# Kernel tuning notes

Measured on AMD Instinct MI355X. Metric: run time of the kernel, lower is better.

Reference implementation:

```python
import jax, jax.numpy as jnp
import numpy as np

HIDDEN = 896
INTER = 2560
N_EXPERTS = 16
TOP_K = 4


def setup_inputs() -> dict:
    key = jax.random.key(0)
    ks = jax.random.split(key, 9)
    s = lambda fan_in: 1.0 / np.sqrt(fan_in)
    x = jax.random.normal(ks[0], (2, 1024, HIDDEN), dtype=jnp.float32)
    router_w = jax.random.normal(ks[1], (HIDDEN, N_EXPERTS), dtype=jnp.float32) * s(HIDDEN)
    # routed experts, stacked: y = x @ W (equivalent to nn.Linear with W.T)
    Wg = jax.random.normal(ks[2], (N_EXPERTS, HIDDEN, INTER), dtype=jnp.float32) * s(HIDDEN)
    Wu = jax.random.normal(ks[3], (N_EXPERTS, HIDDEN, INTER), dtype=jnp.float32) * s(HIDDEN)
    Wd = jax.random.normal(ks[4], (N_EXPERTS, INTER, HIDDEN), dtype=jnp.float32) * s(INTER)
    # single shared expert
    Sg = jax.random.normal(ks[5], (HIDDEN, INTER), dtype=jnp.float32) * s(HIDDEN)
    Su = jax.random.normal(ks[6], (HIDDEN, INTER), dtype=jnp.float32) * s(HIDDEN)
    Sd = jax.random.normal(ks[7], (INTER, HIDDEN), dtype=jnp.float32) * s(INTER)
    return {"x": x, "router_w": router_w, "Wg": Wg, "Wu": Wu, "Wd": Wd,
            "Sg": Sg, "Su": Su, "Sd": Sd}


def reference(x, router_w, Wg, Wu, Wd, Sg, Su, Sd):
    B, N, D = x.shape
    xf = x.reshape(-1, D)  # [T, D]

    # shared expert (all tokens): SwiGLU
    shared = (jax.nn.silu(xf @ Sg) * (xf @ Su)) @ Sd  # [T, D]

    # router: softmax -> top-k -> renormalize
    logits = xf @ router_w                      # [T, E]
    probs = jax.nn.softmax(logits, axis=-1)
    top_v, top_i = jax.lax.top_k(probs, TOP_K)  # [T, K]
    w = top_v / (top_v.sum(axis=-1, keepdims=True) + 1e-8)

    # load-balance loss
    one_hot = jax.nn.one_hot(top_i, N_EXPERTS, dtype=probs.dtype)  # [T, K, E]
    f = one_hot.sum(axis=1).mean(axis=0)   # fraction routed per expert
    P = probs.mean(axis=0)                 # mean router prob per expert
    balance_loss = N_EXPERTS * (f * P).sum()

    # dense-dispatch combine weights [T, E] (zero for unselected experts)
    combine = (w[..., None] * one_hot).sum(axis=1)  # [T, E]

    # all-expert SwiGLU, combined with per-token routing weights
    g = jnp.einsum('td,edi->tei', xf, Wg)
    u = jnp.einsum('td,edi->tei', xf, Wu)
    h = jax.nn.silu(g) * u                          # [T, E, I]
    routed = jnp.einsum('tei,eid,te->td', h, Wd, combine)

    out = (routed + shared).reshape(B, N, D)
    return out, balance_loss
```

## Files before the change

### kernel.cpp

```cpp
#include <hip/hip_runtime.h>
#include <hip/hip_bf16.h>


#define T_TOK 2048
#define DIM   896
#define INTERN 2560
#define NEXP  16
#define TOPK  4
#define MT    64
#define IC    256
#define ICAP  133

#define SLOTGU ((size_t)80 * 56 * 512)
#define SLOTD  ((size_t)28 * 160 * 512)

typedef __attribute__((ext_vector_type(8)))  __bf16 bf16x8;
typedef __attribute__((ext_vector_type(4)))  __bf16 bf16x4;
typedef __attribute__((ext_vector_type(16))) float  f32x16;

__device__ __forceinline__ void panel_barrier() {
  asm volatile("s_waitcnt lgkmcnt(0)" ::: "memory");
  __builtin_amdgcn_s_barrier();
  __builtin_amdgcn_sched_barrier(0);
}

__device__ __forceinline__ bool decode_work(const int* cnt, int b, int idx,
                                            int& g, int& tile) {
  int K0 = (cnt[b] + MT - 1) >> 6;
  int K1 = (cnt[b + 8] + MT - 1) >> 6;
  if (idx < K0) { g = b; tile = idx; return true; }
  idx -= K0;
  if (idx < K1) { g = b + 8; tile = idx; return true; }
  idx -= K1;
  if (idx < 4) { g = NEXP; tile = b + 8 * idx; return true; }
  return false;
}

__global__ void router_k(const float* __restrict__ x, const float* __restrict__ rw,
                         int* __restrict__ cnt, float* __restrict__ Pacc,
                         float* __restrict__ facc, int* __restrict__ tok,
                         float* __restrict__ wts) {
  int lane = threadIdx.x & 63;
  int t = blockIdx.x * 4 + (threadIdx.x >> 6);
  const float* xr = x + (size_t)t * DIM;

  float acc[NEXP];
#pragma unroll
  for (int e = 0; e < NEXP; ++e) acc[e] = 0.f;
  for (int i = 0; i < DIM / 64; ++i) {
    int d = i * 64 + lane;
    float xv = xr[d];
    const float* r = rw + d * NEXP;
#pragma unroll
    for (int e = 0; e < NEXP; ++e) acc[e] = fmaf(xv, r[e], acc[e]);
  }
#pragma unroll
  for (int e = 0; e < NEXP; ++e) {
    float v = acc[e];
    v += __shfl_xor(v, 32); v += __shfl_xor(v, 16); v += __shfl_xor(v, 8);
    v += __shfl_xor(v, 4);  v += __shfl_xor(v, 2);  v += __shfl_xor(v, 1);
    acc[e] = v;
  }
  float m = acc[0];
#pragma unroll
  for (int e = 1; e < NEXP; ++e) m = fmaxf(m, acc[e]);
  float p[NEXP]; float s = 0.f;
#pragma unroll
  for (int e = 0; e < NEXP; ++e) { p[e] = __expf(acc[e] - m); s += p[e]; }
  float is = 1.f / s;
#pragma unroll
  for (int e = 0; e < NEXP; ++e) p[e] *= is;

  float pc[NEXP];
#pragma unroll
  for (int e = 0; e < NEXP; ++e) pc[e] = p[e];
  int sels[TOPK]; float svs[TOPK]; float s4 = 0.f;
#pragma unroll
  for (int k = 0; k < TOPK; ++k) {
    int best = 0; float bv = pc[0];
#pragma unroll
    for (int e = 1; e < NEXP; ++e) { if (pc[e] > bv) { bv = pc[e]; best = e; } }
    sels[k] = best; svs[k] = bv; s4 += bv;
#pragma unroll
    for (int e = 0; e < NEXP; ++e) { if (e == best) pc[e] = -1.f; }
  }
  float inv = 1.f / (s4 + 1e-8f);

  if (lane < NEXP) atomicAdd(&Pacc[lane], p[lane] * (1.f / T_TOK));
  if (lane < TOPK) {
    int e = sels[lane]; float w = svs[lane] * inv;
    atomicAdd(&facc[e], 1.f / T_TOK);
    int pos = atomicAdd(&cnt[e], 1);
    tok[e * T_TOK + pos] = t;
    wts[e * T_TOK + pos] = w;
  }
}

__global__ void loss_k(const float* __restrict__ Pacc, const float* __restrict__ facc,
                       const int* __restrict__ cnt, int* __restrict__ offs,
                       float* __restrict__ dst) {
  if (threadIdx.x == 0) {
    float s = 0.f;
    for (int e = 0; e < NEXP; ++e) s += Pacc[e] * facc[e];
    *dst = (float)NEXP * s;
    int o = 0;
    for (int e = 0; e < NEXP; ++e) { offs[e] = o; o += cnt[e]; }
    offs[NEXP] = o;
  }
}

__global__ __launch_bounds__(256, 8) void packall_k(
    const float* __restrict__ Wg, const float* __restrict__ Sg,
    __hip_bfloat16* __restrict__ PG,
    const float* __restrict__ Wu, const float* __restrict__ Su,
    __hip_bfloat16* __restrict__ PU,
    const float* __restrict__ Wd, const float* __restrict__ Sd,
    __hip_bfloat16* __restrict__ PD) {
  int bid = blockIdx.x;
  int which = bid / 9520;
  int r = bid % 9520;
  int z = r / 560, rr = r % 560;
  int K, N, kt, nt;
  const float *srcE, *srcS; __hip_bfloat16* dst;
  if (which < 2) {
    K = DIM; N = INTERN; kt = rr % 14; nt = rr / 14;
    srcE = which ? Wu : Wg; srcS = which ? Su : Sg; dst = which ? PU : PG;
  } else {
    K = INTERN; N = DIM; kt = rr % 40; nt = rr / 40;
    srcE = Wd; srcS = Sd; dst = PD;
  }
  const float* src = (z < NEXP) ? srcE + (size_t)z * K * N : srcS;
  __hip_bfloat16* d = dst + (size_t)z * ((size_t)(K >> 4) * (N >> 5) * 512);

  __shared__ float tile[64][65];
  int tid = threadIdx.x;
  int r0 = tid >> 4, c4 = (tid & 15) << 2;
  const float* s = src + (size_t)(kt * 64) * N + nt * 64;
#pragma unroll
  for (int it = 0; it < 4; ++it) {
    int rw_ = r0 + 16 * it;
    float4 v = *reinterpret_cast<const float4*>(s + (size_t)rw_ * N + c4);
    tile[rw_][c4] = v.x; tile[rw_][c4 + 1] = v.y;
    tile[rw_][c4 + 2] = v.z; tile[rw_][c4 + 3] = v.w;
  }
  __syncthreads();
  int lane = tid & 63, h5 = lane >> 5, c31 = lane & 31;
  int KS = K >> 4;
#pragma unroll
  for (int it = 0; it < 2; ++it) {
    int cc = (tid >> 6) + 4 * it;
    int nbl = cc >> 2, ksl = cc & 3;
    bf16x8 v;
#pragma unroll
    for (int e = 0; e < 8; ++e)
      v[e] = (__bf16)tile[ksl * 16 + 8 * h5 + e][nbl * 32 + c31];
    size_t n_blk = (size_t)nt * 2 + nbl, ks = (size_t)kt * 4 + ksl;
    *reinterpret_cast<bf16x8*>(d + ((n_blk * KS + ks) * 64 + lane) * 8) = v;
  }
}

__global__ __launch_bounds__(512, 4) void h4_k(
    const float* __restrict__ x, const int* __restrict__ cnt,
    const int* __restrict__ offs, const int* __restrict__ tok,
    const __hip_bfloat16* __restrict__ PG, const __hip_bfloat16* __restrict__ PU,
    __hip_bfloat16* __restrict__ H) {
  int bid = blockIdx.x;
  int ch = bid / (8 * ICAP);
  int r_ = bid % (8 * ICAP);
  int b = r_ & 7, idx = r_ >> 3;
  int g, tile;
  if (!decode_work(cnt, b, idx, g, tile)) return;
  int M = (g < NEXP) ? cnt[g] : T_TOK;
  int m0 = tile * MT;

  __shared__ int rows_s[MT];
  __shared__ __align__(16) char xph[32768];
  char (*xp)[16384] = reinterpret_cast<char (*)[16384]>(xph);
  char* hb = xph;

  int tid = threadIdx.x;
  if (tid < MT) {
    if (g < NEXP) {
      int i = m0 + tid;
      rows_s[tid] = tok[g * T_TOK + ((i < M) ? i : m0)];
    } else rows_s[tid] = m0 + tid;
  }
  __syncthreads();

  int wv = tid >> 6, lane = tid & 63;
  int h5 = lane >> 5, c31 = lane & 31;

  int srow = tid >> 3, sc8 = tid & 7;
  const float* xr = x + (size_t)rows_s[srow] * DIM;
  int sswz = (srow & 7) << 4;

#define LDX(p, j) (*reinterpret_cast<const float4*>(xr + (p) * 128 + (sc8 + 8 * (j)) * 4))
#define STX(pb, j, v) { bf16x4 _b; _b[0]=(__bf16)(v).x; _b[1]=(__bf16)(v).y; \
    _b[2]=(__bf16)(v).z; _b[3]=(__bf16)(v).w; \
    *reinterpret_cast<bf16x4*>(&xp[pb][(srow * 256 + sc8 * 8 + 64 * (j)) ^ sswz]) = _b; }
#define XF(pb, row, ksl) (*reinterpret_cast<const bf16x8*>( \
    &xp[pb][((row) * 256 + (ksl) * 32 + h5 * 16) ^ (((row) & 7) << 4)]))

  int slot = (g < NEXP) ? g : NEXP;
  const __hip_bfloat16* bg = PG + (size_t)slot * SLOTGU +
      ((size_t)(ch * 8 + wv) * 56) * 512 + lane * 8;
  const __hip_bfloat16* bu = PU + (size_t)slot * SLOTGU +
      ((size_t)(ch * 8 + wv) * 56) * 512 + lane * 8;

  bf16x8 g0 = *reinterpret_cast<const bf16x8*>(bg);
  bf16x8 g1 = *reinterpret_cast<const bf16x8*>(bg + 512);
  bf16x8 g2 = *reinterpret_cast<const bf16x8*>(bg + 1024);
  bf16x8 g3 = *reinterpret_cast<const bf16x8*>(bg + 1536);
  bf16x8 u0 = *reinterpret_cast<const bf16x8*>(bu);
  bf16x8 u1 = *reinterpret_cast<const bf16x8*>(bu + 512);
  bf16x8 u2 = *reinterpret_cast<const bf16x8*>(bu + 1024);
  bf16x8 u3 = *reinterpret_cast<const bf16x8*>(bu + 1536);

  {
    float4 a0 = LDX(0, 0), a1 = LDX(0, 1), a2 = LDX(0, 2), a3 = LDX(0, 3);
    STX(0, 0, a0) STX(0, 1, a1) STX(0, 2, a2) STX(0, 3, a3)
  }
  panel_barrier();

  f32x16 ag0, ag1, au0, au1;
#pragma unroll
  for (int r = 0; r < 16; ++r) { ag0[r] = 0.f; ag1[r] = 0.f; au0[r] = 0.f; au1[r] = 0.f; }

#define STEP(S, GB, UB) { \
    bf16x8 xa = XF(pb, c31, S), xb = XF(pb, c31 + 32, S); \
    ag0 = __builtin_amdgcn_mfma_f32_32x32x16_bf16(GB, xa, ag0, 0, 0, 0); \
    ag1 = __builtin_amdgcn_mfma_f32_32x32x16_bf16(GB, xb, ag1, 0, 0, 0); \
    au0 = __builtin_amdgcn_mfma_f32_32x32x16_bf16(UB, xa, au0, 0, 0, 0); \
    au1 = __builtin_amdgcn_mfma_f32_32x32x16_bf16(UB, xb, au1, 0, 0, 0); \
    int nk = 8 * p + (S) + 4; if (nk >= 56) nk = 0; \
    GB = *reinterpret_cast<const bf16x8*>(bg + (size_t)nk * 512); \
    UB = *reinterpret_cast<const bf16x8*>(bu + (size_t)nk * 512); }

  float4 s0, s1, s2, s3;
  for (int p = 0; p < 7; ++p) {
    int pb = p & 1;
    if (p < 6) { s0 = LDX(p + 1, 0); s1 = LDX(p + 1, 1); }
    STEP(0, g0, u0) STEP(1, g1, u1) STEP(2, g2, u2)
    if (p < 6) {
      STX(pb ^ 1, 0, s0) STX(pb ^ 1, 1, s1)
      s2 = LDX(p + 1, 2); s3 = LDX(p + 1, 3);
    }
    STEP(3, g3, u3) STEP(4, g0, u0) STEP(5, g1, u1)
    if (p < 6) { STX(pb ^ 1, 2, s2) STX(pb ^ 1, 3, s3) }
    STEP(6, g2, u2) STEP(7, g3, u3)
    panel_barrier();
  }
#undef STEP

#pragma unroll
  for (int mh = 0; mh < 2; ++mh) {
    int tokr = c31 + 32 * mh;
#pragma unroll
    for (int q = 0; q < 4; ++q) {
      bf16x4 hq;
#pragma unroll
      for (int j = 0; j < 4; ++j) {
        float gg = mh ? ag1[4 * q + j] : ag0[4 * q + j];
        float uu = mh ? au1[4 * q + j] : au0[4 * q + j];
        hq[j] = (__bf16)(gg / (1.f + __expf(-gg)) * uu);
      }
      int i0 = wv * 32 + 8 * q + 4 * h5;
      int byte = (tokr * 512 + i0 * 2) ^ ((tokr & 7) << 4);
      *reinterpret_cast<bf16x4*>(&hb[byte]) = hq;
    }
  }
  panel_barrier();

  if (g == NEXP || m0 + srow < M) {
    int slotr = offs[g] + m0 + srow;
    __hip_bfloat16* hrow = H + (size_t)slotr * INTERN + ch * IC + sc8 * 32;
#pragma unroll
    for (int qq = 0; qq < 4; ++qq) {
      int byte = (srow * 512 + sc8 * 64 + qq * 16) ^ sswz;
      *reinterpret_cast<bf16x8*>(hrow + qq * 8) =
          *reinterpret_cast<const bf16x8*>(&hb[byte]);
    }
  }
#undef LDX
#undef STX
#undef XF
}

__global__ __launch_bounds__(512, 4) void g24_k(
    const int* __restrict__ cnt, const int* __restrict__ offs,
    const int* __restrict__ tok, const float* __restrict__ wts,
    const __hip_bfloat16* __restrict__ H,
    const __hip_bfloat16* __restrict__ PD, float* __restrict__ out) {
  int bid = blockIdx.x;
  int ns = bid / (8 * ICAP);
  int r_ = bid % (8 * ICAP);
  int b = r_ & 7, idx = r_ >> 3;
  int g, tile;
  if (!decode_work(cnt, b, idx, g, tile)) return;
  int M = (g < NEXP) ? cnt[g] : T_TOK;
  int m0 = tile * MT;

  __shared__ int rows_s[MT];
  __shared__ float w_s[MT];
  __shared__ __align__(16) char hp[2][16384];

  int tid = threadIdx.x;
  if (tid < MT) {
    if (g < NEXP) {
      int i = m0 + tid; bool v = i < M;
      rows_s[tid] = tok[g * T_TOK + (v ? i : m0)];
      w_s[tid]   = v ? wts[g * T_TOK + i] : 0.f;
    } else { rows_s[tid] = m0 + tid; w_s[tid] = 1.f; }
  }
  __syncthreads();

  int wv = tid >> 6, lane = tid & 63, h5 = lane >> 5, c31 = lane & 31;
  int mh = wv & 1, ng = wv >> 1;
  int col = ns * 128 + ng * 32 + c31;

  int slot = (g < NEXP) ? g : NEXP;
  const __hip_bfloat16* bd = PD + (size_t)slot * SLOTD +
      ((size_t)(ns * 4 + ng) * 160) * 512 + lane * 8;

  int slot0 = offs[g] + m0;
  const __hip_bfloat16* Hb = H + (size_t)slot0 * INTERN;

  int srow = tid >> 3, sc8 = tid & 7;
  const __hip_bfloat16* hr = Hb + (size_t)srow * INTERN + sc8 * 16;
  int sswz = (srow & 7) << 4;

  bf16x8 w0 = *reinterpret_cast<const bf16x8*>(bd);
  bf16x8 w1 = *reinterpret_cast<const bf16x8*>(bd + 512);
  bf16x8 w2 = *reinterpret_cast<const bf16x8*>(bd + 1024);
  bf16x8 w3 = *reinterpret_cast<const bf16x8*>(bd + 1536);
  bf16x8 w4 = *reinterpret_cast<const bf16x8*>(bd + 2048);
  bf16x8 w5 = *reinterpret_cast<const bf16x8*>(bd + 2560);
  bf16x8 w6 = *reinterpret_cast<const bf16x8*>(bd + 3072);
  bf16x8 w7 = *reinterpret_cast<const bf16x8*>(bd + 3584);

  bf16x8 t0 = *reinterpret_cast<const bf16x8*>(hr);
  bf16x8 t1 = *reinterpret_cast<const bf16x8*>(hr + 8);
  {
    int b0 = srow * 256 + sc8 * 32;
    *reinterpret_cast<bf16x8*>(&hp[0][b0 ^ sswz]) = t0;
    *reinterpret_cast<bf16x8*>(&hp[0][(b0 + 16) ^ sswz]) = t1;
  }
  panel_barrier();

  f32x16 o;
#pragma unroll
  for (int r = 0; r < 16; ++r) o[r] = 0.f;

  int arow = mh * 32 + c31;
  int aswz = (arow & 7) << 4;

#define G2STEP(KSL, WB) { \
    bf16x8 hf = *reinterpret_cast<const bf16x8*>( \
        &hp[pb][(arow * 256 + (KSL) * 32 + h5 * 16) ^ aswz]); \
    o = __builtin_amdgcn_mfma_f32_32x32x16_bf16(hf, WB, o, 0, 0, 0); \
    int tn = 8 * p + (KSL) + 8; if (tn >= 160) tn -= 160; \
    WB = *reinterpret_cast<const bf16x8*>(bd + (size_t)tn * 512); }

  for (int p = 0; p < 20; ++p) {
    int pb = p & 1;
    if (p < 19) {
      t0 = *reinterpret_cast<const bf16x8*>(hr + (p + 1) * 128);
      t1 = *reinterpret_cast<const bf16x8*>(hr + (p + 1) * 128 + 8);
    }
    G2STEP(0, w0) G2STEP(1, w1) G2STEP(2, w2) G2STEP(3, w3)
    G2STEP(4, w4) G2STEP(5, w5) G2STEP(6, w6) G2STEP(7, w7)
    if (p < 19) {
      int b0 = srow * 256 + sc8 * 32;
      *reinterpret_cast<bf16x8*>(&hp[pb ^ 1][b0 ^ sswz]) = t0;
      *reinterpret_cast<bf16x8*>(&hp[pb ^ 1][(b0 + 16) ^ sswz]) = t1;
    }
    panel_barrier();
  }
#undef G2STEP

#pragma unroll
  for (int r = 0; r < 16; ++r) {
    int row = (r & 3) + 8 * (r >> 2) + 4 * h5 + 32 * mh;
    atomicAdd(&out[(size_t)rows_s[row] * DIM + col], o[r] * w_s[row]);
  }
}

extern "C" void kernel_launch(void* const* d_in, const int* in_sizes, int n_in,
                              void* d_out, int out_size, void* d_ws, size_t ws_size,
                              hipStream_t stream) {
  const float* x  = (const float*)d_in[0];
  const float* rw = (const float*)d_in[1];
  const float* Wg = (const float*)d_in[2];
  const float* Wu = (const float*)d_in[3];
  const float* Wd = (const float*)d_in[4];
  const float* Sg = (const float*)d_in[5];
  const float* Su = (const float*)d_in[6];
  const float* Sd = (const float*)d_in[7];
  float* out = (float*)d_out;

  char* ws = (char*)d_ws;
  int*   cnt  = (int*)ws;
  float* Pacc = (float*)(ws + 64);
  float* facc = (float*)(ws + 128);
  int*   offs = (int*)(ws + 192);
  int*   tok  = (int*)(ws + 320);
  float* wts  = (float*)(ws + 320 + 131072);
  const size_t H_OFF = 262656;
  __hip_bfloat16* H = (__hip_bfloat16*)(ws + H_OFF);
  const size_t H_BYTES = (size_t)(2 * T_TOK * TOPK + T_TOK) * INTERN * 2;

  const size_t PG_OFF = H_OFF + H_BYTES;
  const size_t PBYTES = (size_t)17 * SLOTGU * 2;
  const size_t PU_OFF = PG_OFF + PBYTES;
  const size_t PD_OFF = PU_OFF + PBYTES;
  __hip_bfloat16* PG = (__hip_bfloat16*)(ws + PG_OFF);
  __hip_bfloat16* PU = (__hip_bfloat16*)(ws + PU_OFF);
  __hip_bfloat16* PD = (__hip_bfloat16*)(ws + PD_OFF);

  hipMemsetAsync(d_ws, 0, 320, stream);
  hipMemsetAsync(d_out, 0, (size_t)(T_TOK * DIM + 1) * sizeof(float), stream);

  router_k<<<T_TOK / 4, 256, 0, stream>>>(x, rw, cnt, Pacc, facc, tok, wts);
  loss_k<<<1, 64, 0, stream>>>(Pacc, facc, cnt, offs, out + (size_t)T_TOK * DIM);
  packall_k<<<28560, 256, 0, stream>>>(Wg, Sg, PG, Wu, Su, PU, Wd, Sd, PD);
  h4_k<<<10 * 8 * ICAP, 512, 0, stream>>>(x, cnt, offs, tok, PG, PU, H);
  g24_k<<<7 * 8 * ICAP, 512, 0, stream>>>(cnt, offs, tok, wts, H, PD, out);
}
```

Baseline: 539.7 us.

## Stream gate/up weights through LDS via direct global-to-LDS loads

The gate/up kernel now loads packed weight fragments with global_load_lds into double-buffered LDS instead of register prefetch. The x panel is restaged in 32-column chunks with padded rows rather than a swizzle. The K loop goes from 7 panels of 8 k-steps to 28 panels of 2 k-steps, with a full vmcnt wait and a barrier every panel. This frees registers and lets the hardware copy weights directly into LDS. In exchange it adds many more barriers, shallower prefetch, and LDS use rises to about 75KB per block, which may limit occupancy.

```diff
diff --git a/kernel.cpp b/kernel.cpp
--- a/kernel.cpp
+++ b/kernel.cpp
@@ -17,6 +17,10 @@
 typedef __attribute__((ext_vector_type(8)))  __bf16 bf16x8;
 typedef __attribute__((ext_vector_type(4)))  __bf16 bf16x4;
 typedef __attribute__((ext_vector_type(16))) float  f32x16;
+
+#define GLD_LDS(GP, LP) __builtin_amdgcn_global_load_lds( \
+    (const __attribute__((address_space(1))) void*)(GP), \
+    (__attribute__((address_space(3))) void*)(LP), 16, 0, 0)
 
 __device__ __forceinline__ void panel_barrier() {
   asm volatile("s_waitcnt lgkmcnt(0)" ::: "memory");
@@ -159,7 +163,7 @@
   }
 }
 
-__global__ __launch_bounds__(512, 4) void h4_k(
+__global__ __launch_bounds__(512, 4) void h5_k(
     const float* __restrict__ x, const int* __restrict__ cnt,
     const int* __restrict__ offs, const int* __restrict__ tok,
     const __hip_bfloat16* __restrict__ PG, const __hip_bfloat16* __restrict__ PU,
@@ -174,9 +178,9 @@
   int m0 = tile * MT;
 
   __shared__ int rows_s[MT];
-  __shared__ __align__(16) char xph[32768];
-  char (*xp)[16384] = reinterpret_cast<char (*)[16384]>(xph);
-  char* hb = xph;
+  __shared__ __align__(16) char wb[2][32768];
+  __shared__ __align__(16) char xb[2][5120];
+  char* hb = &wb[0][0];
 
   int tid = threadIdx.x;
   if (tid < MT) {
@@ -189,17 +193,8 @@
 
   int wv = tid >> 6, lane = tid & 63;
   int h5 = lane >> 5, c31 = lane & 31;
-
   int srow = tid >> 3, sc8 = tid & 7;
   const float* xr = x + (size_t)rows_s[srow] * DIM;
-  int sswz = (srow & 7) << 4;
-
-#define LDX(p, j) (*reinterpret_cast<const float4*>(xr + (p) * 128 + (sc8 + 8 * (j)) * 4))
-#define STX(pb, j, v) { bf16x4 _b; _b[0]=(__bf16)(v).x; _b[1]=(__bf16)(v).y; \
-    _b[2]=(__bf16)(v).z; _b[3]=(__bf16)(v).w; \
-    *reinterpret_cast<bf16x4*>(&xp[pb][(srow * 256 + sc8 * 8 + 64 * (j)) ^ sswz]) = _b; }
-#define XF(pb, row, ksl) (*reinterpret_cast<const bf16x8*>( \
-    &xp[pb][((row) * 256 + (ksl) * 32 + h5 * 16) ^ (((row) & 7) << 4)]))
 
   int slot = (g < NEXP) ? g : NEXP;
   const __hip_bfloat16* bg = PG + (size_t)slot * SLOTGU +
@@ -207,50 +202,55 @@
   const __hip_bfloat16* bu = PU + (size_t)slot * SLOTGU +
       ((size_t)(ch * 8 + wv) * 56) * 512 + lane * 8;
 
-  bf16x8 g0 = *reinterpret_cast<const bf16x8*>(bg);
-  bf16x8 g1 = *reinterpret_cast<const bf16x8*>(bg + 512);
-  bf16x8 g2 = *reinterpret_cast<const bf16x8*>(bg + 1024);
-  bf16x8 g3 = *reinterpret_cast<const bf16x8*>(bg + 1536);
-  bf16x8 u0 = *reinterpret_cast<const bf16x8*>(bu);
-  bf16x8 u1 = *reinterpret_cast<const bf16x8*>(bu + 512);
-  bf16x8 u2 = *reinterpret_cast<const bf16x8*>(bu + 1024);
-  bf16x8 u3 = *reinterpret_cast<const bf16x8*>(bu + 1536);
-
-  {
-    float4 a0 = LDX(0, 0), a1 = LDX(0, 1), a2 = LDX(0, 2), a3 = LDX(0, 3);
-    STX(0, 0, a0) STX(0, 1, a1) STX(0, 2, a2) STX(0, 3, a3)
-  }
+#define ISSUE_W(PB, P) { \
+    char* wdst = &wb[PB][wv * 4096]; \
+    const __hip_bfloat16* gg_ = bg + (size_t)(2 * (P)) * 512; \
+    const __hip_bfloat16* gu_ = bu + (size_t)(2 * (P)) * 512; \
+    GLD_LDS(gg_,       wdst); \
+    GLD_LDS(gg_ + 512, wdst + 1024); \
+    GLD_LDS(gu_,       wdst + 2048); \
+    GLD_LDS(gu_ + 512, wdst + 3072); }
+
+#define KSTEP(PB, KSL) { \
+    bf16x8 wg = *reinterpret_cast<const bf16x8*>(&wb[PB][wv * 4096 + (KSL) * 1024 + lane * 16]); \
+    bf16x8 wu = *reinterpret_cast<const bf16x8*>(&wb[PB][wv * 4096 + 2048 + (KSL) * 1024 + lane * 16]); \
+    bf16x8 xa = *reinterpret_cast<const bf16x8*>(&xb[PB][c31 * 80 + (KSL) * 32 + h5 * 16]); \
+    bf16x8 xc = *reinterpret_cast<const bf16x8*>(&xb[PB][(c31 + 32) * 80 + (KSL) * 32 + h5 * 16]); \
+    ag0 = __builtin_amdgcn_mfma_f32_32x32x16_bf16(wg, xa, ag0, 0, 0, 0); \
+    ag1 = __builtin_amdgcn_mfma_f32_32x32x16_bf16(wg, xc, ag1, 0, 0, 0); \
+    au0 = __builtin_amdgcn_mfma_f32_32x32x16_bf16(wu, xa, au0, 0, 0, 0); \
+    au1 = __builtin_amdgcn_mfma_f32_32x32x16_bf16(wu, xc, au1, 0, 0, 0); }
+
+#define STX_X(PB, V) { bf16x4 b4_; \
+    b4_[0] = (__bf16)(V).x; b4_[1] = (__bf16)(V).y; \
+    b4_[2] = (__bf16)(V).z; b4_[3] = (__bf16)(V).w; \
+    *reinterpret_cast<bf16x4*>(&xb[PB][srow * 80 + sc8 * 8]) = b4_; }
+
+  f32x16 ag0, ag1, au0, au1;
+#pragma unroll
+  for (int r = 0; r < 16; ++r) { ag0[r] = 0.f; ag1[r] = 0.f; au0[r] = 0.f; au1[r] = 0.f; }
+
+  float4 xv;
+  ISSUE_W(0, 0)
+  xv = *reinterpret_cast<const float4*>(xr + sc8 * 4);
+  asm volatile("s_waitcnt vmcnt(0)" ::: "memory");
+  STX_X(0, xv)
   panel_barrier();
 
-  f32x16 ag0, ag1, au0, au1;
-#pragma unroll
-  for (int r = 0; r < 16; ++r) { ag0[r] = 0.f; ag1[r] = 0.f; au0[r] = 0.f; au1[r] = 0.f; }
-
-#define STEP(S, GB, UB) { \
-    bf16x8 xa = XF(pb, c31, S), xb = XF(pb, c31 + 32, S); \
-    ag0 = __builtin_amdgcn_mfma_f32_32x32x16_bf16(GB, xa, ag0, 0, 0, 0); \
-    ag1 = __builtin_amdgcn_mfma_f32_32x32x16_bf16(GB, xb, ag1, 0, 0, 0); \
-    au0 = __builtin_amdgcn_mfma_f32_32x32x16_bf16(UB, xa, au0, 0, 0, 0); \
-    au1 = __builtin_amdgcn_mfma_f32_32x32x16_bf16(UB, xb, au1, 0, 0, 0); \
-    int nk = 8 * p + (S) + 4; if (nk >= 56) nk = 0; \
-    GB = *reinterpret_cast<const bf16x8*>(bg + (size_t)nk * 512); \
-    UB = *reinterpret_cast<const bf16x8*>(bu + (size_t)nk * 512); }
-
-  float4 s0, s1, s2, s3;
-  for (int p = 0; p < 7; ++p) {
+  for (int p = 0; p < 28; ++p) {
     int pb = p & 1;
-    if (p < 6) { s0 = LDX(p + 1, 0); s1 = LDX(p + 1, 1); }
-    STEP(0, g0, u0) STEP(1, g1, u1) STEP(2, g2, u2)
-    if (p < 6) {
-      STX(pb ^ 1, 0, s0) STX(pb ^ 1, 1, s1)
-      s2 = LDX(p + 1, 2); s3 = LDX(p + 1, 3);
+    if (p < 27) {
+      ISSUE_W(pb ^ 1, p + 1)
+      xv = *reinterpret_cast<const float4*>(xr + (p + 1) * 32 + sc8 * 4);
     }
-    STEP(3, g3, u3) STEP(4, g0, u0) STEP(5, g1, u1)
-    if (p < 6) { STX(pb ^ 1, 2, s2) STX(pb ^ 1, 3, s3) }
-    STEP(6, g2, u2) STEP(7, g3, u3)
+    KSTEP(pb, 0) KSTEP(pb, 1)
+    asm volatile("s_waitcnt vmcnt(0)" ::: "memory");
+    if (p < 27) STX_X(pb ^ 1, xv)
     panel_barrier();
   }
-#undef STEP
+#undef ISSUE_W
+#undef KSTEP
+#undef STX_X
 
 #pragma unroll
   for (int mh = 0; mh < 2; ++mh) {
@@ -273,6 +273,7 @@
 
   if (g == NEXP || m0 + srow < M) {
     int slotr = offs[g] + m0 + srow;
+    int sswz = (srow & 7) << 4;
     __hip_bfloat16* hrow = H + (size_t)slotr * INTERN + ch * IC + sc8 * 32;
 #pragma unroll
     for (int qq = 0; qq < 4; ++qq) {
@@ -281,9 +282,6 @@
           *reinterpret_cast<const bf16x8*>(&hb[byte]);
     }
   }
-#undef LDX
-#undef STX
-#undef XF
 }
 
 __global__ __launch_bounds__(512, 4) void g24_k(
@@ -423,6 +421,6 @@
   router_k<<<T_TOK / 4, 256, 0, stream>>>(x, rw, cnt, Pacc, facc, tok, wts);
   loss_k<<<1, 64, 0, stream>>>(Pacc, facc, cnt, offs, out + (size_t)T_TOK * DIM);
   packall_k<<<28560, 256, 0, stream>>>(Wg, Sg, PG, Wu, Su, PU, Wd, Sd, PD);
-  h4_k<<<10 * 8 * ICAP, 512, 0, stream>>>(x, cnt, offs, tok, PG, PU, H);
+  h5_k<<<10 * 8 * ICAP, 512, 0, stream>>>(x, cnt, offs, tok, PG, PU, H);
   g24_k<<<7 * 8 * ICAP, 512, 0, stream>>>(cnt, offs, tok, wts, H, PD, out);
 }
```

Measured after the change: 547.8 us. No clear change (+1.5%).

## Retile expert GEMMs to 128-token tiles with narrower intermediate chunks

Applied to the files above, without the earlier changes.

Both expert GEMM kernels now process 128-token tiles instead of 64. Waves are split into two token halves, and the gate/up kernel covers 128 intermediate columns per block instead of 256. The aim is to reuse each packed weight fragment across twice as many tokens, which halves weight traffic per token. The cost is more registers per wave (occupancy bound lowered to 3), more padding waste on partially filled expert tiles, and more K iterations each with a barrier.

```diff
diff --git a/kernel.cpp b/kernel.cpp
--- a/kernel.cpp
+++ b/kernel.cpp
@@ -7,9 +7,8 @@
 #define INTERN 2560
 #define NEXP  16
 #define TOPK  4
-#define MT    64
-#define IC    256
-#define ICAP  133
+#define MT    128
+#define ICAP  37
 
 #define SLOTGU ((size_t)80 * 56 * 512)
 #define SLOTD  ((size_t)28 * 160 * 512)
@@ -17,6 +16,15 @@
 typedef __attribute__((ext_vector_type(8)))  __bf16 bf16x8;
 typedef __attribute__((ext_vector_type(4)))  __bf16 bf16x4;
 typedef __attribute__((ext_vector_type(16))) float  f32x16;
+
+#define MFMA32(A, B, C) __builtin_amdgcn_mfma_f32_32x32x16_bf16(A, B, C, 0, 0, 0)
+
+__device__ __forceinline__ bf16x8 pack8(float4 a, float4 b) {
+  bf16x8 r;
+  r[0] = (__bf16)a.x; r[1] = (__bf16)a.y; r[2] = (__bf16)a.z; r[3] = (__bf16)a.w;
+  r[4] = (__bf16)b.x; r[5] = (__bf16)b.y; r[6] = (__bf16)b.z; r[7] = (__bf16)b.w;
+  return r;
+}
 
 __device__ __forceinline__ void panel_barrier() {
   asm volatile("s_waitcnt lgkmcnt(0)" ::: "memory");
@@ -26,13 +34,13 @@
 
 __device__ __forceinline__ bool decode_work(const int* cnt, int b, int idx,
                                             int& g, int& tile) {
-  int K0 = (cnt[b] + MT - 1) >> 6;
-  int K1 = (cnt[b + 8] + MT - 1) >> 6;
+  int K0 = (cnt[b] + MT - 1) >> 7;
+  int K1 = (cnt[b + 8] + MT - 1) >> 7;
   if (idx < K0) { g = b; tile = idx; return true; }
   idx -= K0;
   if (idx < K1) { g = b + 8; tile = idx; return true; }
   idx -= K1;
-  if (idx < 4) { g = NEXP; tile = b + 8 * idx; return true; }
+  if (idx < 2) { g = NEXP; tile = b + 8 * idx; return true; }
   return false;
 }
 
@@ -159,7 +167,7 @@
   }
 }
 
-__global__ __launch_bounds__(512, 4) void h4_k(
+__global__ __launch_bounds__(512, 3) void h8_k(
     const float* __restrict__ x, const int* __restrict__ cnt,
     const int* __restrict__ offs, const int* __restrict__ tok,
     const __hip_bfloat16* __restrict__ PG, const __hip_bfloat16* __restrict__ PU,
@@ -189,36 +197,46 @@
 
   int wv = tid >> 6, lane = tid & 63;
   int h5 = lane >> 5, c31 = lane & 31;
-
-  int srow = tid >> 3, sc8 = tid & 7;
+  int ig = wv & 3, th = wv >> 2;
+
+  int srow = tid >> 2, sc4 = tid & 3;
   const float* xr = x + (size_t)rows_s[srow] * DIM;
   int sswz = (srow & 7) << 4;
 
-#define LDX(p, j) (*reinterpret_cast<const float4*>(xr + (p) * 128 + (sc8 + 8 * (j)) * 4))
-#define STX(pb, j, v) { bf16x4 _b; _b[0]=(__bf16)(v).x; _b[1]=(__bf16)(v).y; \
-    _b[2]=(__bf16)(v).z; _b[3]=(__bf16)(v).w; \
-    *reinterpret_cast<bf16x4*>(&xp[pb][(srow * 256 + sc8 * 8 + 64 * (j)) ^ sswz]) = _b; }
+#define LDX(p, j) (*reinterpret_cast<const float4*>(xr + (p) * 64 + sc4 * 16 + (j) * 4))
+#define STXA(pb, v0, v1) { \
+    *reinterpret_cast<bf16x8*>(&xp[pb][(srow * 128 + sc4 * 32) ^ sswz]) = pack8(v0, v1); }
+#define STXB(pb, v2, v3) { \
+    *reinterpret_cast<bf16x8*>(&xp[pb][(srow * 128 + sc4 * 32 + 16) ^ sswz]) = pack8(v2, v3); }
 #define XF(pb, row, ksl) (*reinterpret_cast<const bf16x8*>( \
-    &xp[pb][((row) * 256 + (ksl) * 32 + h5 * 16) ^ (((row) & 7) << 4)]))
+    &xp[pb][((row) * 128 + (ksl) * 32 + h5 * 16) ^ (((row) & 7) << 4)]))
 
   int slot = (g < NEXP) ? g : NEXP;
   const __hip_bfloat16* bg = PG + (size_t)slot * SLOTGU +
-      ((size_t)(ch * 8 + wv) * 56) * 512 + lane * 8;
+      ((size_t)(ch * 4 + ig) * 56) * 512 + lane * 8;
   const __hip_bfloat16* bu = PU + (size_t)slot * SLOTGU +
-      ((size_t)(ch * 8 + wv) * 56) * 512 + lane * 8;
+      ((size_t)(ch * 4 + ig) * 56) * 512 + lane * 8;
 
   bf16x8 g0 = *reinterpret_cast<const bf16x8*>(bg);
   bf16x8 g1 = *reinterpret_cast<const bf16x8*>(bg + 512);
   bf16x8 g2 = *reinterpret_cast<const bf16x8*>(bg + 1024);
   bf16x8 g3 = *reinterpret_cast<const bf16x8*>(bg + 1536);
+  bf16x8 g4 = *reinterpret_cast<const bf16x8*>(bg + 2048);
+  bf16x8 g5 = *reinterpret_cast<const bf16x8*>(bg + 2560);
+  bf16x8 g6 = *reinterpret_cast<const bf16x8*>(bg + 3072);
+  bf16x8 g7 = *reinterpret_cast<const bf16x8*>(bg + 3584);
   bf16x8 u0 = *reinterpret_cast<const bf16x8*>(bu);
   bf16x8 u1 = *reinterpret_cast<const bf16x8*>(bu + 512);
   bf16x8 u2 = *reinterpret_cast<const bf16x8*>(bu + 1024);
   bf16x8 u3 = *reinterpret_cast<const bf16x8*>(bu + 1536);
+  bf16x8 u4 = *reinterpret_cast<const bf16x8*>(bu + 2048);
+  bf16x8 u5 = *reinterpret_cast<const bf16x8*>(bu + 2560);
+  bf16x8 u6 = *reinterpret_cast<const bf16x8*>(bu + 3072);
+  bf16x8 u7 = *reinterpret_cast<const bf16x8*>(bu + 3584);
 
   {
     float4 a0 = LDX(0, 0), a1 = LDX(0, 1), a2 = LDX(0, 2), a3 = LDX(0, 3);
-    STX(0, 0, a0) STX(0, 1, a1) STX(0, 2, a2) STX(0, 3, a3)
+    STXA(0, a0, a1) STXB(0, a2, a3)
   }
   panel_barrier();
 
@@ -227,45 +245,46 @@
   for (int r = 0; r < 16; ++r) { ag0[r] = 0.f; ag1[r] = 0.f; au0[r] = 0.f; au1[r] = 0.f; }
 
 #define STEP(S, GB, UB) { \
-    bf16x8 xa = XF(pb, c31, S), xb = XF(pb, c31 + 32, S); \
-    ag0 = __builtin_amdgcn_mfma_f32_32x32x16_bf16(GB, xa, ag0, 0, 0, 0); \
-    ag1 = __builtin_amdgcn_mfma_f32_32x32x16_bf16(GB, xb, ag1, 0, 0, 0); \
-    au0 = __builtin_amdgcn_mfma_f32_32x32x16_bf16(UB, xa, au0, 0, 0, 0); \
-    au1 = __builtin_amdgcn_mfma_f32_32x32x16_bf16(UB, xb, au1, 0, 0, 0); \
-    int nk = 8 * p + (S) + 4; if (nk >= 56) nk = 0; \
+    bf16x8 xa = XF(pb, th * 64 + c31, S), xb = XF(pb, th * 64 + 32 + c31, S); \
+    ag0 = MFMA32(GB, xa, ag0); ag1 = MFMA32(GB, xb, ag1); \
+    au0 = MFMA32(UB, xa, au0); au1 = MFMA32(UB, xb, au1); \
+    int nk = 4 * p + (S) + 8; if (nk >= 56) nk = 0; \
     GB = *reinterpret_cast<const bf16x8*>(bg + (size_t)nk * 512); \
     UB = *reinterpret_cast<const bf16x8*>(bu + (size_t)nk * 512); }
 
   float4 s0, s1, s2, s3;
-  for (int p = 0; p < 7; ++p) {
+  for (int p = 0; p < 14; ++p) {
     int pb = p & 1;
-    if (p < 6) { s0 = LDX(p + 1, 0); s1 = LDX(p + 1, 1); }
-    STEP(0, g0, u0) STEP(1, g1, u1) STEP(2, g2, u2)
-    if (p < 6) {
-      STX(pb ^ 1, 0, s0) STX(pb ^ 1, 1, s1)
+    if (p < 13) { s0 = LDX(p + 1, 0); s1 = LDX(p + 1, 1); }
+    if (p & 1) { STEP(0, g4, u4) STEP(1, g5, u5) }
+    else       { STEP(0, g0, u0) STEP(1, g1, u1) }
+    if (p < 13) {
       s2 = LDX(p + 1, 2); s3 = LDX(p + 1, 3);
-    }
-    STEP(3, g3, u3) STEP(4, g0, u0) STEP(5, g1, u1)
-    if (p < 6) { STX(pb ^ 1, 2, s2) STX(pb ^ 1, 3, s3) }
-    STEP(6, g2, u2) STEP(7, g3, u3)
+      STXA(pb ^ 1, s0, s1)
+    }
+    if (p & 1) { STEP(2, g6, u6) }
+    else       { STEP(2, g2, u2) }
+    if (p < 13) STXB(pb ^ 1, s2, s3)
+    if (p & 1) { STEP(3, g7, u7) }
+    else       { STEP(3, g3, u3) }
     panel_barrier();
   }
 #undef STEP
 
 #pragma unroll
-  for (int mh = 0; mh < 2; ++mh) {
-    int tokr = c31 + 32 * mh;
+  for (int tgl = 0; tgl < 2; ++tgl) {
+    int tokr = th * 64 + tgl * 32 + c31;
 #pragma unroll
     for (int q = 0; q < 4; ++q) {
       bf16x4 hq;
 #pragma unroll
       for (int j = 0; j < 4; ++j) {
-        float gg = mh ? ag1[4 * q + j] : ag0[4 * q + j];
-        float uu = mh ? au1[4 * q + j] : au0[4 * q + j];
+        float gg = tgl ? ag1[4 * q + j] : ag0[4 * q + j];
+        float uu = tgl ? au1[4 * q + j] : au0[4 * q + j];
         hq[j] = (__bf16)(gg / (1.f + __expf(-gg)) * uu);
       }
-      int i0 = wv * 32 + 8 * q + 4 * h5;
-      int byte = (tokr * 512 + i0 * 2) ^ ((tokr & 7) << 4);
+      int i0 = ig * 32 + 8 * q + 4 * h5;
+      int byte = (tokr * 256 + i0 * 2) ^ ((tokr & 7) << 4);
       *reinterpret_cast<bf16x4*>(&hb[byte]) = hq;
     }
   }
@@ -273,20 +292,21 @@
 
   if (g == NEXP || m0 + srow < M) {
     int slotr = offs[g] + m0 + srow;
-    __hip_bfloat16* hrow = H + (size_t)slotr * INTERN + ch * IC + sc8 * 32;
+    __hip_bfloat16* hrow = H + (size_t)slotr * INTERN + ch * 128 + sc4 * 32;
 #pragma unroll
     for (int qq = 0; qq < 4; ++qq) {
-      int byte = (srow * 512 + sc8 * 64 + qq * 16) ^ sswz;
+      int byte = (srow * 256 + sc4 * 64 + qq * 16) ^ sswz;
       *reinterpret_cast<bf16x8*>(hrow + qq * 8) =
           *reinterpret_cast<const bf16x8*>(&hb[byte]);
     }
   }
 #undef LDX
-#undef STX
+#undef STXA
+#undef STXB
 #undef XF
 }
 
-__global__ __launch_bounds__(512, 4) void g24_k(
+__global__ __launch_bounds__(512, 3) void g28_k(
     const int* __restrict__ cnt, const int* __restrict__ offs,
     const int* __restrict__ tok, const float* __restrict__ wts,
     const __hip_bfloat16* __restrict__ H,
@@ -315,18 +335,16 @@
   __syncthreads();
 
   int wv = tid >> 6, lane = tid & 63, h5 = lane >> 5, c31 = lane & 31;
-  int mh = wv & 1, ng = wv >> 1;
-  int col = ns * 128 + ng * 32 + c31;
+  int cg = wv & 3, th = wv >> 2;
+  int col = ns * 128 + cg * 32 + c31;
 
   int slot = (g < NEXP) ? g : NEXP;
   const __hip_bfloat16* bd = PD + (size_t)slot * SLOTD +
-      ((size_t)(ns * 4 + ng) * 160) * 512 + lane * 8;
+      ((size_t)(ns * 4 + cg) * 160) * 512 + lane * 8;
 
   int slot0 = offs[g] + m0;
-  const __hip_bfloat16* Hb = H + (size_t)slot0 * INTERN;
-
-  int srow = tid >> 3, sc8 = tid & 7;
-  const __hip_bfloat16* hr = Hb + (size_t)srow * INTERN + sc8 * 16;
+  int srow = tid >> 2, sc4 = tid & 3;
+  const __hip_bfloat16* hr = H + (size_t)(slot0 + srow) * INTERN + sc4 * 16;
   int sswz = (srow & 7) << 4;
 
   bf16x8 w0 = *reinterpret_cast<const bf16x8*>(bd);
@@ -341,47 +359,54 @@
   bf16x8 t0 = *reinterpret_cast<const bf16x8*>(hr);
   bf16x8 t1 = *reinterpret_cast<const bf16x8*>(hr + 8);
   {
-    int b0 = srow * 256 + sc8 * 32;
+    int b0 = srow * 128 + sc4 * 32;
     *reinterpret_cast<bf16x8*>(&hp[0][b0 ^ sswz]) = t0;
     *reinterpret_cast<bf16x8*>(&hp[0][(b0 + 16) ^ sswz]) = t1;
   }
   panel_barrier();
 
-  f32x16 o;
-#pragma unroll
-  for (int r = 0; r < 16; ++r) o[r] = 0.f;
-
-  int arow = mh * 32 + c31;
-  int aswz = (arow & 7) << 4;
-
-#define G2STEP(KSL, WB) { \
-    bf16x8 hf = *reinterpret_cast<const bf16x8*>( \
-        &hp[pb][(arow * 256 + (KSL) * 32 + h5 * 16) ^ aswz]); \
-    o = __builtin_amdgcn_mfma_f32_32x32x16_bf16(hf, WB, o, 0, 0, 0); \
-    int tn = 8 * p + (KSL) + 8; if (tn >= 160) tn -= 160; \
+  f32x16 o0, o1;
+#pragma unroll
+  for (int r = 0; r < 16; ++r) { o0[r] = 0.f; o1[r] = 0.f; }
+
+#define HPF(pb, row, ksl) (*reinterpret_cast<const bf16x8*>( \
+    &hp[pb][((row) * 128 + (ksl) * 32 + h5 * 16) ^ (((row) & 7) << 4)]))
+
+#define G2STEP(S, WB) { \
+    bf16x8 ha = HPF(pb, th * 64 + c31, S); \
+    bf16x8 hc = HPF(pb, th * 64 + 32 + c31, S); \
+    o0 = MFMA32(ha, WB, o0); o1 = MFMA32(hc, WB, o1); \
+    int tn = 4 * p + (S) + 8; if (tn >= 160) tn = 0; \
     WB = *reinterpret_cast<const bf16x8*>(bd + (size_t)tn * 512); }
 
-  for (int p = 0; p < 20; ++p) {
+  for (int p = 0; p < 40; ++p) {
     int pb = p & 1;
-    if (p < 19) {
-      t0 = *reinterpret_cast<const bf16x8*>(hr + (p + 1) * 128);
-      t1 = *reinterpret_cast<const bf16x8*>(hr + (p + 1) * 128 + 8);
-    }
-    G2STEP(0, w0) G2STEP(1, w1) G2STEP(2, w2) G2STEP(3, w3)
-    G2STEP(4, w4) G2STEP(5, w5) G2STEP(6, w6) G2STEP(7, w7)
-    if (p < 19) {
-      int b0 = srow * 256 + sc8 * 32;
+    if (p < 39) {
+      t0 = *reinterpret_cast<const bf16x8*>(hr + (p + 1) * 64);
+      t1 = *reinterpret_cast<const bf16x8*>(hr + (p + 1) * 64 + 8);
+    }
+    if (p & 1) { G2STEP(0, w4) G2STEP(1, w5) }
+    else       { G2STEP(0, w0) G2STEP(1, w1) }
+    if (p < 39) {
+      int b0 = srow * 128 + sc4 * 32;
       *reinterpret_cast<bf16x8*>(&hp[pb ^ 1][b0 ^ sswz]) = t0;
       *reinterpret_cast<bf16x8*>(&hp[pb ^ 1][(b0 + 16) ^ sswz]) = t1;
     }
+    if (p & 1) { G2STEP(2, w6) G2STEP(3, w7) }
+    else       { G2STEP(2, w2) G2STEP(3, w3) }
     panel_barrier();
   }
 #undef G2STEP
-
-#pragma unroll
-  for (int r = 0; r < 16; ++r) {
-    int row = (r & 3) + 8 * (r >> 2) + 4 * h5 + 32 * mh;
-    atomicAdd(&out[(size_t)rows_s[row] * DIM + col], o[r] * w_s[row]);
+#undef HPF
+
+#pragma unroll
+  for (int tgl = 0; tgl < 2; ++tgl) {
+#pragma unroll
+    for (int r = 0; r < 16; ++r) {
+      int row = th * 64 + tgl * 32 + (r & 3) + 8 * (r >> 2) + 4 * h5;
+      float v = (tgl ? o1[r] : o0[r]) * w_s[row];
+      atomicAdd(&out[(size_t)rows_s[row] * DIM + col], v);
+    }
   }
 }
 
@@ -423,6 +448,6 @@
   router_k<<<T_TOK / 4, 256, 0, stream>>>(x, rw, cnt, Pacc, facc, tok, wts);
   loss_k<<<1, 64, 0, stream>>>(Pacc, facc, cnt, offs, out + (size_t)T_TOK * DIM);
   packall_k<<<28560, 256, 0, stream>>>(Wg, Sg, PG, Wu, Su, PU, Wd, Sd, PD);
-  h4_k<<<10 * 8 * ICAP, 512, 0, stream>>>(x, cnt, offs, tok, PG, PU, H);
-  g24_k<<<7 * 8 * ICAP, 512, 0, stream>>>(cnt, offs, tok, wts, H, PD, out);
-}
+  h8_k<<<20 * 8 * ICAP, 512, 0, stream>>>(x, cnt, offs, tok, PG, PU, H);
+  g28_k<<<7 * 8 * ICAP, 512, 0, stream>>>(cnt, offs, tok, wts, H, PD, out);
+}
```

After: 1.568 ms. 190% more time.

## Make gate/up kernel weight-stationary with LDS-resident weight slices looping over all tokens

Applied to the files above, without the earlier changes.

The gate/up projection kernel is restructured so that each block owns one expert and one 32-column slice of the intermediate dimension. It loads the full 896x32 gate and up weight panels into LDS once, then loops over that expert's tokens in tiles of 256. This replaces the old layout, where many 64-token tiles each reread the weights from global memory, and is meant to cut repeated weight traffic. In exchange the launch drops to 1360 blocks of 256 threads using about 150KB of LDS, so occupancy is one block per CU. Each token tile also converts x to bf16 in a serialized panel loop with two barriers per panel, and blocks for heavily loaded experts run longer, which risks load imbalance.

```diff
diff --git a/kernel.cpp b/kernel.cpp
--- a/kernel.cpp
+++ b/kernel.cpp
@@ -8,7 +8,6 @@
 #define NEXP  16
 #define TOPK  4
 #define MT    64
-#define IC    256
 #define ICAP  133
 
 #define SLOTGU ((size_t)80 * 56 * 512)
@@ -17,6 +16,15 @@
 typedef __attribute__((ext_vector_type(8)))  __bf16 bf16x8;
 typedef __attribute__((ext_vector_type(4)))  __bf16 bf16x4;
 typedef __attribute__((ext_vector_type(16))) float  f32x16;
+
+#define MFMA32(A, B, C) __builtin_amdgcn_mfma_f32_32x32x16_bf16(A, B, C, 0, 0, 0)
+
+__device__ __forceinline__ bf16x8 pack8(float4 a, float4 b) {
+  bf16x8 r;
+  r[0] = (__bf16)a.x; r[1] = (__bf16)a.y; r[2] = (__bf16)a.z; r[3] = (__bf16)a.w;
+  r[4] = (__bf16)b.x; r[5] = (__bf16)b.y; r[6] = (__bf16)b.z; r[7] = (__bf16)b.w;
+  return r;
+}
 
 __device__ __forceinline__ void panel_barrier() {
   asm volatile("s_waitcnt lgkmcnt(0)" ::: "memory");
@@ -159,131 +167,106 @@
   }
 }
 
-__global__ __launch_bounds__(512, 4) void h4_k(
+__global__ __launch_bounds__(256, 1) void h9_k(
     const float* __restrict__ x, const int* __restrict__ cnt,
     const int* __restrict__ offs, const int* __restrict__ tok,
     const __hip_bfloat16* __restrict__ PG, const __hip_bfloat16* __restrict__ PU,
     __hip_bfloat16* __restrict__ H) {
   int bid = blockIdx.x;
-  int ch = bid / (8 * ICAP);
-  int r_ = bid % (8 * ICAP);
-  int b = r_ & 7, idx = r_ >> 3;
-  int g, tile;
-  if (!decode_work(cnt, b, idx, g, tile)) return;
+  int g = bid % 17, nc = bid / 17;
   int M = (g < NEXP) ? cnt[g] : T_TOK;
-  int m0 = tile * MT;
-
-  __shared__ int rows_s[MT];
-  __shared__ __align__(16) char xph[32768];
-  char (*xp)[16384] = reinterpret_cast<char (*)[16384]>(xph);
-  char* hb = xph;
+
+  __shared__ int rows_s[256];
+  __shared__ __align__(16) char wg[57344];
+  __shared__ __align__(16) char wu[57344];
+  __shared__ __align__(16) char xpan[32768];
 
   int tid = threadIdx.x;
-  if (tid < MT) {
-    if (g < NEXP) {
-      int i = m0 + tid;
-      rows_s[tid] = tok[g * T_TOK + ((i < M) ? i : m0)];
-    } else rows_s[tid] = m0 + tid;
-  }
-  __syncthreads();
-
   int wv = tid >> 6, lane = tid & 63;
   int h5 = lane >> 5, c31 = lane & 31;
-
-  int srow = tid >> 3, sc8 = tid & 7;
-  const float* xr = x + (size_t)rows_s[srow] * DIM;
-  int sswz = (srow & 7) << 4;
-
-#define LDX(p, j) (*reinterpret_cast<const float4*>(xr + (p) * 128 + (sc8 + 8 * (j)) * 4))
-#define STX(pb, j, v) { bf16x4 _b; _b[0]=(__bf16)(v).x; _b[1]=(__bf16)(v).y; \
-    _b[2]=(__bf16)(v).z; _b[3]=(__bf16)(v).w; \
-    *reinterpret_cast<bf16x4*>(&xp[pb][(srow * 256 + sc8 * 8 + 64 * (j)) ^ sswz]) = _b; }
-#define XF(pb, row, ksl) (*reinterpret_cast<const bf16x8*>( \
-    &xp[pb][((row) * 256 + (ksl) * 32 + h5 * 16) ^ (((row) & 7) << 4)]))
-
-  int slot = (g < NEXP) ? g : NEXP;
-  const __hip_bfloat16* bg = PG + (size_t)slot * SLOTGU +
-      ((size_t)(ch * 8 + wv) * 56) * 512 + lane * 8;
-  const __hip_bfloat16* bu = PU + (size_t)slot * SLOTGU +
-      ((size_t)(ch * 8 + wv) * 56) * 512 + lane * 8;
-
-  bf16x8 g0 = *reinterpret_cast<const bf16x8*>(bg);
-  bf16x8 g1 = *reinterpret_cast<const bf16x8*>(bg + 512);
-  bf16x8 g2 = *reinterpret_cast<const bf16x8*>(bg + 1024);
-  bf16x8 g3 = *reinterpret_cast<const bf16x8*>(bg + 1536);
-  bf16x8 u0 = *reinterpret_cast<const bf16x8*>(bu);
-  bf16x8 u1 = *reinterpret_cast<const bf16x8*>(bu + 512);
-  bf16x8 u2 = *reinterpret_cast<const bf16x8*>(bu + 1024);
-  bf16x8 u3 = *reinterpret_cast<const bf16x8*>(bu + 1536);
+  int wbase = wv * 64;
 
   {
-    float4 a0 = LDX(0, 0), a1 = LDX(0, 1), a2 = LDX(0, 2), a3 = LDX(0, 3);
-    STX(0, 0, a0) STX(0, 1, a1) STX(0, 2, a2) STX(0, 3, a3)
-  }
-  panel_barrier();
-
-  f32x16 ag0, ag1, au0, au1;
-#pragma unroll
-  for (int r = 0; r < 16; ++r) { ag0[r] = 0.f; ag1[r] = 0.f; au0[r] = 0.f; au1[r] = 0.f; }
-
-#define STEP(S, GB, UB) { \
-    bf16x8 xa = XF(pb, c31, S), xb = XF(pb, c31 + 32, S); \
-    ag0 = __builtin_amdgcn_mfma_f32_32x32x16_bf16(GB, xa, ag0, 0, 0, 0); \
-    ag1 = __builtin_amdgcn_mfma_f32_32x32x16_bf16(GB, xb, ag1, 0, 0, 0); \
-    au0 = __builtin_amdgcn_mfma_f32_32x32x16_bf16(UB, xa, au0, 0, 0, 0); \
-    au1 = __builtin_amdgcn_mfma_f32_32x32x16_bf16(UB, xb, au1, 0, 0, 0); \
-    int nk = 8 * p + (S) + 4; if (nk >= 56) nk = 0; \
-    GB = *reinterpret_cast<const bf16x8*>(bg + (size_t)nk * 512); \
-    UB = *reinterpret_cast<const bf16x8*>(bu + (size_t)nk * 512); }
-
-  float4 s0, s1, s2, s3;
-  for (int p = 0; p < 7; ++p) {
-    int pb = p & 1;
-    if (p < 6) { s0 = LDX(p + 1, 0); s1 = LDX(p + 1, 1); }
-    STEP(0, g0, u0) STEP(1, g1, u1) STEP(2, g2, u2)
-    if (p < 6) {
-      STX(pb ^ 1, 0, s0) STX(pb ^ 1, 1, s1)
-      s2 = LDX(p + 1, 2); s3 = LDX(p + 1, 3);
-    }
-    STEP(3, g3, u3) STEP(4, g0, u0) STEP(5, g1, u1)
-    if (p < 6) { STX(pb ^ 1, 2, s2) STX(pb ^ 1, 3, s3) }
-    STEP(6, g2, u2) STEP(7, g3, u3)
-    panel_barrier();
-  }
-#undef STEP
-
-#pragma unroll
-  for (int mh = 0; mh < 2; ++mh) {
-    int tokr = c31 + 32 * mh;
-#pragma unroll
-    for (int q = 0; q < 4; ++q) {
-      bf16x4 hq;
-#pragma unroll
-      for (int j = 0; j < 4; ++j) {
-        float gg = mh ? ag1[4 * q + j] : ag0[4 * q + j];
-        float uu = mh ? au1[4 * q + j] : au0[4 * q + j];
-        hq[j] = (__bf16)(gg / (1.f + __expf(-gg)) * uu);
+    const bf16x8* pgs = reinterpret_cast<const bf16x8*>(
+        PG + (size_t)g * SLOTGU + (size_t)nc * 56 * 512);
+    const bf16x8* pus = reinterpret_cast<const bf16x8*>(
+        PU + (size_t)g * SLOTGU + (size_t)nc * 56 * 512);
+    bf16x8* wg8 = reinterpret_cast<bf16x8*>(wg);
+    bf16x8* wu8 = reinterpret_cast<bf16x8*>(wu);
+    for (int i = tid; i < 3584; i += 256) { wg8[i] = pgs[i]; wu8[i] = pus[i]; }
+  }
+
+  int ntile = (M + 255) >> 8;
+  for (int tt = 0; tt < ntile; ++tt) {
+    {
+      int i = tt * 256 + tid;
+      if (g < NEXP) rows_s[tid] = tok[g * T_TOK + ((i < M) ? i : tt * 256)];
+      else          rows_s[tid] = i;
+    }
+    __syncthreads();
+    const float* xr = x + (size_t)rows_s[tid] * DIM;
+
+    f32x16 ag0, ag1, au0, au1;
+#pragma unroll
+    for (int r = 0; r < 16; ++r) { ag0[r] = 0.f; ag1[r] = 0.f; au0[r] = 0.f; au1[r] = 0.f; }
+
+    for (int pan = 0; pan < 14; ++pan) {
+#pragma unroll
+      for (int j = 0; j < 8; ++j) {
+        float4 a = *reinterpret_cast<const float4*>(xr + pan * 64 + j * 8);
+        float4 b = *reinterpret_cast<const float4*>(xr + pan * 64 + j * 8 + 4);
+        *reinterpret_cast<bf16x8*>(&xpan[(tid * 128 + j * 16) ^ ((tid & 7) << 4)]) =
+            pack8(a, b);
       }
-      int i0 = wv * 32 + 8 * q + 4 * h5;
-      int byte = (tokr * 512 + i0 * 2) ^ ((tokr & 7) << 4);
-      *reinterpret_cast<bf16x4*>(&hb[byte]) = hq;
-    }
-  }
-  panel_barrier();
-
-  if (g == NEXP || m0 + srow < M) {
-    int slotr = offs[g] + m0 + srow;
-    __hip_bfloat16* hrow = H + (size_t)slotr * INTERN + ch * IC + sc8 * 32;
-#pragma unroll
-    for (int qq = 0; qq < 4; ++qq) {
-      int byte = (srow * 512 + sc8 * 64 + qq * 16) ^ sswz;
-      *reinterpret_cast<bf16x8*>(hrow + qq * 8) =
-          *reinterpret_cast<const bf16x8*>(&hb[byte]);
-    }
-  }
-#undef LDX
-#undef STX
-#undef XF
+      __syncthreads();
+#pragma unroll
+      for (int ksl = 0; ksl < 4; ++ksl) {
+        int ks = pan * 4 + ksl;
+        bf16x8 a_g = *reinterpret_cast<const bf16x8*>(&wg[ks * 1024 + lane * 16]);
+        bf16x8 a_u = *reinterpret_cast<const bf16x8*>(&wu[ks * 1024 + lane * 16]);
+        int r0 = wbase + c31, r1 = wbase + 32 + c31;
+        bf16x8 b0 = *reinterpret_cast<const bf16x8*>(
+            &xpan[(r0 * 128 + ksl * 32 + h5 * 16) ^ ((r0 & 7) << 4)]);
+        bf16x8 b1 = *reinterpret_cast<const bf16x8*>(
+            &xpan[(r1 * 128 + ksl * 32 + h5 * 16) ^ ((r1 & 7) << 4)]);
+        ag0 = MFMA32(a_g, b0, ag0); ag1 = MFMA32(a_g, b1, ag1);
+        au0 = MFMA32(a_u, b0, au0); au1 = MFMA32(a_u, b1, au1);
+      }
+      __syncthreads();
+    }
+
+#pragma unroll
+    for (int half = 0; half < 2; ++half) {
+      int tokr = wbase + half * 32 + c31;
+#pragma unroll
+      for (int q = 0; q < 4; ++q) {
+        bf16x4 hq;
+#pragma unroll
+        for (int j = 0; j < 4; ++j) {
+          float gg = half ? ag1[4 * q + j] : ag0[4 * q + j];
+          float uu = half ? au1[4 * q + j] : au0[4 * q + j];
+          hq[j] = (__bf16)(gg / (1.f + __expf(-gg)) * uu);
+        }
+        int byte = (tokr * 64 + (8 * q + 4 * h5) * 2) ^ ((tokr & 3) << 4);
+        *reinterpret_cast<bf16x4*>(&xpan[byte]) = hq;
+      }
+    }
+    __syncthreads();
+
+    {
+      int i = tt * 256 + tid;
+      if (i < M) {
+        int slotr = offs[g] + i;
+        __hip_bfloat16* hrow = H + (size_t)slotr * INTERN + nc * 32;
+#pragma unroll
+        for (int q = 0; q < 4; ++q)
+          *reinterpret_cast<bf16x8*>(hrow + q * 8) =
+              *reinterpret_cast<const bf16x8*>(
+                  &xpan[(tid * 64 + q * 16) ^ ((tid & 3) << 4)]);
+      }
+    }
+    __syncthreads();
+  }
 }
 
 __global__ __launch_bounds__(512, 4) void g24_k(
@@ -423,6 +406,6 @@
   router_k<<<T_TOK / 4, 256, 0, stream>>>(x, rw, cnt, Pacc, facc, tok, wts);
   loss_k<<<1, 64, 0, stream>>>(Pacc, facc, cnt, offs, out + (size_t)T_TOK * DIM);
   packall_k<<<28560, 256, 0, stream>>>(Wg, Sg, PG, Wu, Su, PU, Wd, Sd, PD);
-  h4_k<<<10 * 8 * ICAP, 512, 0, stream>>>(x, cnt, offs, tok, PG, PU, H);
+  h9_k<<<17 * 80, 256, 0, stream>>>(x, cnt, offs, tok, PG, PU, H);
   g24_k<<<7 * 8 * ICAP, 512, 0, stream>>>(cnt, offs, tok, wts, H, PD, out);
 }
```

Measured after the change: 1.170 ms. +116.8%, slower.
